# Performance work log

Measured on AMD Instinct MI355X. Metric: run time of the kernel, lower is better.

The kernel has to match this reference:

```python
import jax, jax.numpy as jnp
import numpy as np
import math

IN_F, OUT_F = 512, 512
N_HEADS, N_SPLITS = 32, 4
N = 1024
DELTA_SCALE = 0.1


def setup_inputs() -> dict:
    key = jax.random.key(0)
    k_x, k_h, k_s, k_w = jax.random.split(key, 4)
    stdv = 1.0 / math.sqrt(OUT_F)
    inputs = {
        "input": jax.random.normal(k_x, (N, IN_F), dtype=jnp.float32),
        "head_ix": jax.random.randint(k_h, (N,), 0, N_HEADS, dtype=jnp.int32),
        "split_ix": jax.random.randint(k_s, (N,), 0, N_SPLITS, dtype=jnp.int32),
        # learned parameters (EmbeddingTensor tables)
        "weight": jax.random.uniform(k_w, (N_HEADS, IN_F, OUT_F), dtype=jnp.float32,
                                     minval=-stdv, maxval=stdv),
        "delta_weight": jnp.zeros((N_HEADS * N_SPLITS, IN_F, OUT_F), dtype=jnp.float32),
        "bias": jnp.zeros((N_HEADS, OUT_F), dtype=jnp.float32),
    }
    return inputs


def reference(input, head_ix, split_ix, weight, delta_weight, bias):
    # per-sample weight: base[head] + 0.1 * delta[head * n_splits + split]
    w = weight[head_ix] + delta_weight[head_ix * N_SPLITS + split_ix] * DELTA_SCALE  # [N, in, out]
    # batched vector-matrix multiply + per-head bias
    return jnp.einsum('ab,abc->ac', input, w) + bias[head_ix]  # [N, out]
```

## Files before the change

kernel.cpp:

```cpp
#include <hip/hip_runtime.h>

#define N_SAMP   1024
#define IN_F     512
#define OUT_F    512
#define N_HEADS  32
#define N_SPLITS 4
#define DELTA_SCALE 0.1f

template <int J, bool DELTA, int NSG, int MINW>
__global__ __launch_bounds__(256, MINW) void lms_stream(
    const float* __restrict__ X, const int* __restrict__ head_ix,
    const int* __restrict__ split_ix, const float* __restrict__ Wt,
    const float* __restrict__ bias, float* __restrict__ out)
{
    constexpr int KQ   = 8;
    constexpr int KT   = IN_F / KQ;
    constexpr int NST  = KT / 4;
    constexpr int NOUT = (J * 32) / 256;

    __shared__ float buf[J * IN_F];
    __shared__ int   list[N_SAMP];
    __shared__ int   wsum[4];

    const int g    = blockIdx.y / NSG;
    const int sg   = blockIdx.y % NSG;
    const int c0   = blockIdx.x * 64;
    const int tid  = threadIdx.x;
    const int c2   = tid & 31;
    const int kq   = tid >> 5;
    const int lane = tid & 63;
    const int wave = tid >> 6;

    int run = 0;
    for (int r = 0; r < N_SAMP / 256; ++r) {
        const int i   = r * 256 + tid;
        const int key = DELTA ? head_ix[i] * N_SPLITS + split_ix[i] : head_ix[i];
        const bool hit = (key == g);
        const unsigned long long m = __ballot(hit);
        if (lane == 0) wsum[wave] = __popcll(m);
        __syncthreads();
        int base = run;
        for (int w = 0; w < 4; ++w)
            if (w < wave) base += wsum[w];
        if (hit)
            list[base + __popcll(m & ((1ULL << lane) - 1ULL))] = i;
        run += wsum[0] + wsum[1] + wsum[2] + wsum[3];
        __syncthreads();
    }
    const int total = run;
    if (total <= sg * J && total > 0) return;
    if (total == 0) return;

    const float* wp = Wt + (size_t)g * (IN_F * OUT_F)
                    + (size_t)(kq * KT) * OUT_F + c0 + c2 * 2;

    for (int s0 = sg * J; s0 < total; s0 += NSG * J) {
        const int nc = min(total - s0, J);

        __syncthreads();
        for (int i = tid; i < J * (IN_F / 4); i += 256) {
            const int s = i >> 7, q = i & 127;
            float4 v = make_float4(0.f, 0.f, 0.f, 0.f);
            if (s < nc)
                v = *(const float4*)(X + (size_t)list[s0 + s] * IN_F + q * 4);
            *(float4*)(&buf[s * IN_F + q * 4]) = v;
        }
        __syncthreads();

        float2 acc[J];
#pragma unroll
        for (int j = 0; j < J; ++j) { acc[j].x = 0.f; acc[j].y = 0.f; }

        float2 rb[2][4];
#pragma unroll
        for (int u = 0; u < 4; ++u)
            rb[0][u] = *(const float2*)(wp + (size_t)u * OUT_F);

#pragma unroll 2
        for (int st = 0; st < NST; ++st) {
            const int nx = (st + 1 < NST) ? st + 1 : NST - 1;
            const float* wn = wp + (size_t)(nx * 4) * OUT_F;
            const int nb = (st + 1) & 1, cb = st & 1;
#pragma unroll
            for (int u = 0; u < 4; ++u)
                rb[nb][u] = *(const float2*)(wn + (size_t)u * OUT_F);

            const float* xb = &buf[kq * KT + st * 4];
#pragma unroll
            for (int j = 0; j < J; ++j) {
                const float4 xv = *(const float4*)(xb + j * IN_F);
                acc[j].x += xv.x * rb[cb][0].x; acc[j].y += xv.x * rb[cb][0].y;
                acc[j].x += xv.y * rb[cb][1].x; acc[j].y += xv.y * rb[cb][1].y;
                acc[j].x += xv.z * rb[cb][2].x; acc[j].y += xv.z * rb[cb][2].y;
                acc[j].x += xv.w * rb[cb][3].x; acc[j].y += xv.w * rb[cb][3].y;
            }
        }

        __syncthreads();
        float2* Red = (float2*)buf;
#pragma unroll
        for (int j = 0; j < J; ++j)
            Red[(kq * J + j) * 32 + c2] = acc[j];
        __syncthreads();

#pragma unroll
        for (int t = 0; t < NOUT; ++t) {
            const int oi = t * 256 + tid;
            const int j = oi >> 5, cc = oi & 31;
            if (j < nc) {
                float2 s = make_float2(0.f, 0.f);
#pragma unroll
                for (int q = 0; q < KQ; ++q) {
                    const float2 r = Red[(q * J + j) * 32 + cc];
                    s.x += r.x; s.y += r.y;
                }
                float* op = out + (size_t)list[s0 + j] * OUT_F + c0 + cc * 2;
                float2 res;
                if (DELTA) {
                    const float2 cur = *(const float2*)op;
                    res.x = cur.x + DELTA_SCALE * s.x;
                    res.y = cur.y + DELTA_SCALE * s.y;
                } else {
                    const float2 bv =
                        *(const float2*)(bias + (size_t)g * OUT_F + c0 + cc * 2);
                    res.x = s.x + bv.x;
                    res.y = s.y + bv.y;
                }
                *(float2*)op = res;
            }
        }
    }
}

extern "C" void kernel_launch(void* const* d_in, const int* in_sizes, int n_in,
                              void* d_out, int out_size, void* d_ws, size_t ws_size,
                              hipStream_t stream) {
    const float* X        = (const float*)d_in[0];
    const int*   head_ix  = (const int*)d_in[1];
    const int*   split_ix = (const int*)d_in[2];
    const float* W        = (const float*)d_in[3];
    const float* D        = (const float*)d_in[4];
    const float* bias     = (const float*)d_in[5];
    float*       out      = (float*)d_out;

    dim3 gb(OUT_F / 64, N_HEADS * 2);
    lms_stream<32, false, 2, 2><<<gb, 256, 0, stream>>>(
        X, head_ix, split_ix, W, bias, out);

    dim3 gd(OUT_F / 64, N_HEADS * N_SPLITS);
    lms_stream<16, true, 1, 4><<<gd, 256, 0, stream>>>(
        X, head_ix, split_ix, D, bias, out);
}
```

Before: 258.9 us.

## Fuse base and delta passes into one interleaved launch with float4 tiles

Merges the base-weight and delta-weight streaming kernels into one launch. Blocks are interleaved one base to two delta so both weight tables stream at the same time. The delta pass writes into a workspace buffer, and a small combine kernel then adds 0.1× of it to the output. Each thread now covers four columns with float4 weight loads, giving 128-column tiles, and the reduction is done in two halves to fit shared memory. The goal is to remove the serialization between the two passes and widen memory accesses. The cost is an extra kernel and a full read-modify-write of the output and workspace.

```diff
diff --git a/kernel.cpp b/kernel.cpp
--- a/kernel.cpp
+++ b/kernel.cpp
@@ -7,29 +7,26 @@
 #define N_SPLITS 4
 #define DELTA_SCALE 0.1f
 
-template <int J, bool DELTA, int NSG, int MINW>
-__global__ __launch_bounds__(256, MINW) void lms_stream(
+__device__ __forceinline__ void fma4(float4& a, float x, const float4& w) {
+    a.x += x * w.x; a.y += x * w.y; a.z += x * w.z; a.w += x * w.w;
+}
+
+template <int J, int NSG, bool DELTA>
+__device__ __forceinline__ void role_pass(
     const float* __restrict__ X, const int* __restrict__ head_ix,
     const int* __restrict__ split_ix, const float* __restrict__ Wt,
-    const float* __restrict__ bias, float* __restrict__ out)
+    const float* __restrict__ bias, float* __restrict__ dst,
+    int g, int tileIdx, int sg, float* buf, int* list, int* wsum)
 {
-    constexpr int KQ   = 8;
-    constexpr int KT   = IN_F / KQ;
-    constexpr int NST  = KT / 4;
-    constexpr int NOUT = (J * 32) / 256;
+    constexpr int KQ  = 8;
+    constexpr int KT  = IN_F / KQ;
+    constexpr int NST = KT / 4;
 
-    __shared__ float buf[J * IN_F];
-    __shared__ int   list[N_SAMP];
-    __shared__ int   wsum[4];
-
-    const int g    = blockIdx.y / NSG;
-    const int sg   = blockIdx.y % NSG;
-    const int c0   = blockIdx.x * 64;
     const int tid  = threadIdx.x;
-    const int c2   = tid & 31;
+    const int lane = tid & 63, wave = tid >> 6;
+    const int ct   = tid & 31;
     const int kq   = tid >> 5;
-    const int lane = tid & 63;
-    const int wave = tid >> 6;
+    const int c0   = tileIdx * 128;
 
     int run = 0;
     for (int r = 0; r < N_SAMP / 256; ++r) {
@@ -48,11 +45,10 @@
         __syncthreads();
     }
     const int total = run;
-    if (total <= sg * J && total > 0) return;
-    if (total == 0) return;
+    if (total == 0 || total <= sg * J) return;
 
     const float* wp = Wt + (size_t)g * (IN_F * OUT_F)
-                    + (size_t)(kq * KT) * OUT_F + c0 + c2 * 2;
+                    + (size_t)(kq * KT) * OUT_F + c0 + ct * 4;
 
     for (int s0 = sg * J; s0 < total; s0 += NSG * J) {
         const int nc = min(total - s0, J);
@@ -67,69 +63,107 @@
         }
         __syncthreads();
 
-        float2 acc[J];
+        float4 acc[J];
 #pragma unroll
-        for (int j = 0; j < J; ++j) { acc[j].x = 0.f; acc[j].y = 0.f; }
+        for (int j = 0; j < J; ++j) acc[j] = make_float4(0.f, 0.f, 0.f, 0.f);
 
-        float2 rb[2][4];
+        float4 rb[2][4];
 #pragma unroll
         for (int u = 0; u < 4; ++u)
-            rb[0][u] = *(const float2*)(wp + (size_t)u * OUT_F);
+            rb[0][u] = *(const float4*)(wp + (size_t)u * OUT_F);
 
-#pragma unroll 2
+        const float* xb = &buf[kq * KT];
         for (int st = 0; st < NST; ++st) {
             const int nx = (st + 1 < NST) ? st + 1 : NST - 1;
+            const int nb = (st + 1) & 1, cb = st & 1;
             const float* wn = wp + (size_t)(nx * 4) * OUT_F;
-            const int nb = (st + 1) & 1, cb = st & 1;
 #pragma unroll
             for (int u = 0; u < 4; ++u)
-                rb[nb][u] = *(const float2*)(wn + (size_t)u * OUT_F);
-
-            const float* xb = &buf[kq * KT + st * 4];
+                rb[nb][u] = *(const float4*)(wn + (size_t)u * OUT_F);
 #pragma unroll
             for (int j = 0; j < J; ++j) {
-                const float4 xv = *(const float4*)(xb + j * IN_F);
-                acc[j].x += xv.x * rb[cb][0].x; acc[j].y += xv.x * rb[cb][0].y;
-                acc[j].x += xv.y * rb[cb][1].x; acc[j].y += xv.y * rb[cb][1].y;
-                acc[j].x += xv.z * rb[cb][2].x; acc[j].y += xv.z * rb[cb][2].y;
-                acc[j].x += xv.w * rb[cb][3].x; acc[j].y += xv.w * rb[cb][3].y;
+                const float4 xv = *(const float4*)(xb + j * IN_F + st * 4);
+                fma4(acc[j], xv.x, rb[cb][0]);
+                fma4(acc[j], xv.y, rb[cb][1]);
+                fma4(acc[j], xv.z, rb[cb][2]);
+                fma4(acc[j], xv.w, rb[cb][3]);
             }
         }
 
         __syncthreads();
-        float2* Red = (float2*)buf;
+        float4* Red = (float4*)buf;
 #pragma unroll
-        for (int j = 0; j < J; ++j)
-            Red[(kq * J + j) * 32 + c2] = acc[j];
-        __syncthreads();
-
+        for (int half = 0; half < 2; ++half) {
+            if ((ct >> 4) == half) {
+                const int cth = ct & 15;
 #pragma unroll
-        for (int t = 0; t < NOUT; ++t) {
-            const int oi = t * 256 + tid;
-            const int j = oi >> 5, cc = oi & 31;
-            if (j < nc) {
-                float2 s = make_float2(0.f, 0.f);
+                for (int j = 0; j < J; ++j)
+                    Red[(kq * J + j) * 16 + cth] = acc[j];
+            }
+            __syncthreads();
+            for (int t = tid; t < J * 16; t += 256) {
+                const int j = t >> 4, cq = t & 15;
+                if (j < nc) {
+                    float4 s = Red[j * 16 + cq];
 #pragma unroll
-                for (int q = 0; q < KQ; ++q) {
-                    const float2 r = Red[(q * J + j) * 32 + cc];
-                    s.x += r.x; s.y += r.y;
+                    for (int q = 1; q < KQ; ++q) {
+                        const float4 r = Red[(q * J + j) * 16 + cq];
+                        s.x += r.x; s.y += r.y; s.z += r.z; s.w += r.w;
+                    }
+                    const int col = c0 + half * 64 + cq * 4;
+                    float* op = dst + (size_t)list[s0 + j] * OUT_F + col;
+                    if (DELTA) {
+                        *(float4*)op = s;
+                    } else {
+                        const float4 bv =
+                            *(const float4*)(bias + (size_t)g * OUT_F + col);
+                        s.x += bv.x; s.y += bv.y; s.z += bv.z; s.w += bv.w;
+                        *(float4*)op = s;
+                    }
                 }
-                float* op = out + (size_t)list[s0 + j] * OUT_F + c0 + cc * 2;
-                float2 res;
-                if (DELTA) {
-                    const float2 cur = *(const float2*)op;
-                    res.x = cur.x + DELTA_SCALE * s.x;
-                    res.y = cur.y + DELTA_SCALE * s.y;
-                } else {
-                    const float2 bv =
-                        *(const float2*)(bias + (size_t)g * OUT_F + c0 + cc * 2);
-                    res.x = s.x + bv.x;
-                    res.y = s.y + bv.y;
-                }
-                *(float2*)op = res;
             }
+            __syncthreads();
         }
     }
+}
+
+__global__ __launch_bounds__(256, 2) void lms_fused(
+    const float* __restrict__ X, const int* __restrict__ head_ix,
+    const int* __restrict__ split_ix, const float* __restrict__ W,
+    const float* __restrict__ D, const float* __restrict__ bias,
+    float* __restrict__ out, float* __restrict__ ws)
+{
+    __shared__ float buf[16384];
+    __shared__ int   list[N_SAMP];
+    __shared__ int   wsum[4];
+
+    const int bid = blockIdx.x;
+    const int r3  = bid % 3;
+    if (r3 == 0) {
+        const int id = bid / 3;
+        const int head = id & 31;
+        const int tile = (id >> 5) & 3;
+        const int sg   = id >> 7;
+        role_pass<32, 2, false>(X, head_ix, split_ix,
+            W, bias, out, head, tile, sg, buf, list, wsum);
+    } else {
+        const int id = (bid / 3) * 2 + (r3 - 1);
+        const int combo = id & 127;
+        const int tile  = id >> 7;
+        role_pass<16, 1, true>(X, head_ix, split_ix,
+            D, bias, ws, combo, tile, 0, buf, list, wsum);
+    }
+}
+
+__global__ __launch_bounds__(256) void combine_kernel(
+    float* __restrict__ out, const float* __restrict__ ws)
+{
+    const int i = blockIdx.x * 256 + threadIdx.x;
+    float4 o = ((float4*)out)[i];
+    const float4 d = ((const float4*)ws)[i];
+    o.x += DELTA_SCALE * d.x; o.y += DELTA_SCALE * d.y;
+    o.z += DELTA_SCALE * d.z; o.w += DELTA_SCALE * d.w;
+    ((float4*)out)[i] = o;
 }
 
 extern "C" void kernel_launch(void* const* d_in, const int* in_sizes, int n_in,
@@ -142,12 +176,8 @@
     const float* D        = (const float*)d_in[4];
     const float* bias     = (const float*)d_in[5];
     float*       out      = (float*)d_out;
+    float*       ws       = (float*)d_ws;
 
-    dim3 gb(OUT_F / 64, N_HEADS * 2);
-    lms_stream<32, false, 2, 2><<<gb, 256, 0, stream>>>(
-        X, head_ix, split_ix, W, bias, out);
-
-    dim3 gd(OUT_F / 64, N_HEADS * N_SPLITS);
-    lms_stream<16, true, 1, 4><<<gd, 256, 0, stream>>>(
-        X, head_ix, split_ix, D, bias, out);
+    lms_fused<<<768, 256, 0, stream>>>(X, head_ix, split_ix, W, D, bias, out, ws);
+    combine_kernel<<<(N_SAMP * OUT_F / 4) / 256, 256, 0, stream>>>(out, ws);
 }
```

Measured after the change: 369.6 us. 42.8% more time.
